# Performance work log

Hardware: AMD Instinct MI355X
Metric: run time of the kernel (lower is better)

The kernel has to match this reference:

```python
import jax, jax.numpy as jnp
import numpy as np

N_NODES = 100000
IN_CH = 256
OUT_CH = 64
N_EDGES = 3200000


def setup_inputs() -> dict:
    key = jax.random.key(0)
    k1, k2, k3, k4 = jax.random.split(key, 4)
    x = jax.random.normal(k1, (N_NODES, IN_CH), dtype=jnp.float32)
    edge_index = jax.random.randint(k2, (2, N_EDGES), 0, N_NODES, dtype=jnp.int64)
    # GCNConv parameters (glorot-style init for W, zeros for bias as in PyG)
    W = jax.random.normal(k3, (IN_CH, OUT_CH), dtype=jnp.float32) / np.sqrt(IN_CH)
    b = jnp.zeros((OUT_CH,), dtype=jnp.float32)
    return {"x": x, "edge_index": edge_index, "W": W, "b": b}


def reference(x, edge_index, W, b):
    N = x.shape[0]
    # --- GCNConv: add self-loops, symmetric degree normalization ---
    loops = jnp.arange(N, dtype=edge_index.dtype)
    src = jnp.concatenate([edge_index[0], loops])  # [E+N]
    dst = jnp.concatenate([edge_index[1], loops])  # [E+N]
    # degree of each target node (edge weights = 1)
    deg = jax.ops.segment_sum(jnp.ones_like(dst, dtype=x.dtype), dst, num_segments=N)
    dinv = jnp.where(deg > 0, jax.lax.rsqrt(deg), 0.0)  # deg^{-1/2}
    norm = dinv[src] * dinv[dst]                        # [E+N]
    # linear transform first (PyG applies lin before propagate)
    h = x @ W                                           # [N, OUT_CH]
    msg = h[src] * norm[:, None]                        # gather + scale
    out = jax.ops.segment_sum(msg, dst, num_segments=N) + b  # scatter-add + bias
    # --- relu + log_softmax ---
    out = jax.nn.relu(out)
    return jax.nn.log_softmax(out, axis=-1)
```

## Files before the change

kernel.cpp:

```cpp
#include <hip/hip_runtime.h>
#include <cstddef>
#include <cstdint>

#define N_NODES 100000
#define IN_CH 256
#define OUT_CH 64
#define N_EDGES 3200000

#define BKT_SHIFT 7
#define BKT_R     128
#define K_BKT     782
#define BKT_CAP   6144
#define T_PART    8192
#define NBLK_PART ((N_EDGES + T_PART - 1) / T_PART)
#define NBLK_GEMM 512
#define N_TILES   (N_NODES / 16)

#define WS_FLAG_OFF   0
#define WS_GCNT_OFF   64
#define WS_DINV_OFF   4096
#define WS_NSE_OFF    404096
#define WS_EDG_OFF    1204224
#define WS_H_OFF      20422656
#define WS_NEED       33222656

#define WSF_DEG_OFF   4096
#define WSF_DINV_OFF  404096
#define WSF_H_OFF     804096

typedef __attribute__((ext_vector_type(8))) short bshort8;
typedef __attribute__((ext_vector_type(4))) float f32x4;
typedef __attribute__((ext_vector_type(4))) unsigned u32x4;

static __device__ __forceinline__ unsigned short f2bf(float f) {
    unsigned u = __builtin_bit_cast(unsigned, f);
    u += 0x7FFFu + ((u >> 16) & 1u);
    return (unsigned short)(u >> 16);
}
static __device__ __forceinline__ float bflo(unsigned u) {
    return __builtin_bit_cast(float, u << 16);
}
static __device__ __forceinline__ float bfhi(unsigned u) {
    return __builtin_bit_cast(float, u & 0xFFFF0000u);
}

__global__ void probe_kernel(const unsigned* __restrict__ ei, int* __restrict__ flag) {
    if (blockIdx.x == 0 && threadIdx.x == 0) {
        int all0 = 1;
        for (int i = 0; i < 16; ++i) all0 &= (ei[2 * i + 1] == 0u);
        *flag = all0;
    }
}

__device__ __forceinline__ int load_idx(const int* ei32, const long long* ei64,
                                        bool is64, long long pos) {
    return is64 ? (int)ei64[pos] : ei32[pos];
}

static __device__ __forceinline__ void gemm_body(char* smem, int gbid, int nblk,
                                                 const float* __restrict__ x,
                                                 const float* __restrict__ W,
                                                 unsigned short* __restrict__ hs) {
    unsigned short (*Wf)[4][64][8] = (unsigned short (*)[4][64][8])smem;
    const int tid = threadIdx.x;
    const int lane = tid & 63;
    const int wv = tid >> 6;

    for (int i = tid; i < 8 * 4 * 64 * 8; i += 256) {
        int kt = i >> 11;
        int rem = i & 2047;
        int ct = rem >> 9;
        int rem2 = rem & 511;
        int l = rem2 >> 3;
        int j = rem2 & 7;
        int kk = kt * 32 + (l >> 4) * 8 + j;
        int cc = ct * 16 + (l & 15);
        ((unsigned short*)Wf)[i] = f2bf(W[(size_t)kk * OUT_CH + cc]);
    }
    __syncthreads();

    const int r16 = lane & 15;
    const int q = lane >> 4;

    for (int t = gbid * 4 + wv; t < N_TILES; t += nblk * 4) {
        const int row0 = t * 16;
        const float* xrow = &x[(size_t)(row0 + r16) * IN_CH + q * 8];
        f32x4 acc[4] = {{0.f,0.f,0.f,0.f},{0.f,0.f,0.f,0.f},
                        {0.f,0.f,0.f,0.f},{0.f,0.f,0.f,0.f}};
        #pragma unroll
        for (int kt = 0; kt < 8; ++kt) {
            float4 x0 = *(const float4*)&xrow[kt * 32];
            float4 x1 = *(const float4*)&xrow[kt * 32 + 4];
            unsigned p0, p1, p2, p3;
            asm("v_cvt_pk_bf16_f32 %0, %1, %2" : "=v"(p0) : "v"(x0.x), "v"(x0.y));
            asm("v_cvt_pk_bf16_f32 %0, %1, %2" : "=v"(p1) : "v"(x0.z), "v"(x0.w));
            asm("v_cvt_pk_bf16_f32 %0, %1, %2" : "=v"(p2) : "v"(x1.x), "v"(x1.y));
            asm("v_cvt_pk_bf16_f32 %0, %1, %2" : "=v"(p3) : "v"(x1.z), "v"(x1.w));
            u32x4 au = {p0, p1, p2, p3};
            bshort8 af = __builtin_bit_cast(bshort8, au);
            #pragma unroll
            for (int ct = 0; ct < 4; ++ct) {
                bshort8 bf = *(const bshort8*)&Wf[kt][ct][lane][0];
                acc[ct] = __builtin_amdgcn_mfma_f32_16x16x32_bf16(af, bf, acc[ct], 0, 0, 0);
            }
        }
        #pragma unroll
        for (int ct = 0; ct < 4; ++ct) {
            #pragma unroll
            for (int r = 0; r < 4; ++r) {
                int row = row0 + q * 4 + r;
                hs[(size_t)row * OUT_CH + ct * 16 + r16] = f2bf(acc[ct][r]);
            }
        }
    }
}

__global__ __launch_bounds__(512) void partition_kernel(const int* __restrict__ ei32,
                                                        const long long* __restrict__ ei64,
                                                        const int* __restrict__ flag,
                                                        unsigned* __restrict__ gcnt,
                                                        unsigned* __restrict__ edg) {
    __shared__ unsigned hist[K_BKT];
    __shared__ unsigned cur[K_BKT];
    const bool is64 = (*flag != 0);
    const int tid = threadIdx.x;
    const int start = blockIdx.x * T_PART;
    const int end   = min(start + T_PART, N_EDGES);
    for (int k = tid; k < K_BKT; k += 512) hist[k] = 0u;
    __syncthreads();
    if (is64) {
        const longlong2* d2 = (const longlong2*)&ei64[N_EDGES];
        for (int i = (start >> 1) + tid; i < (end >> 1); i += 512) {
            longlong2 d = d2[i];
            atomicAdd(&hist[(int)d.x >> BKT_SHIFT], 1u);
            atomicAdd(&hist[(int)d.y >> BKT_SHIFT], 1u);
        }
    } else {
        const int2* d2 = (const int2*)&ei32[N_EDGES];
        for (int i = (start >> 1) + tid; i < (end >> 1); i += 512) {
            int2 d = d2[i];
            atomicAdd(&hist[d.x >> BKT_SHIFT], 1u);
            atomicAdd(&hist[d.y >> BKT_SHIFT], 1u);
        }
    }
    __syncthreads();
    for (int k = tid; k < K_BKT; k += 512) {
        unsigned c = hist[k];
        unsigned base = c ? atomicAdd(&gcnt[k], c) : 0u;
        cur[k] = base + (unsigned)k * BKT_CAP;
    }
    __syncthreads();
    if (is64) {
        const longlong2* s2 = (const longlong2*)&ei64[0];
        const longlong2* d2 = (const longlong2*)&ei64[N_EDGES];
        for (int i = (start >> 1) + tid; i < (end >> 1); i += 512) {
            longlong2 s = s2[i];
            longlong2 d = d2[i];
            unsigned p0 = atomicAdd(&cur[(int)d.x >> BKT_SHIFT], 1u);
            edg[p0] = (unsigned)s.x | ((unsigned)((int)d.x & (BKT_R - 1)) << 17);
            unsigned p1 = atomicAdd(&cur[(int)d.y >> BKT_SHIFT], 1u);
            edg[p1] = (unsigned)s.y | ((unsigned)((int)d.y & (BKT_R - 1)) << 17);
        }
    } else {
        const int2* s2 = (const int2*)&ei32[0];
        const int2* d2 = (const int2*)&ei32[N_EDGES];
        for (int i = (start >> 1) + tid; i < (end >> 1); i += 512) {
            int2 s = s2[i];
            int2 d = d2[i];
            unsigned p0 = atomicAdd(&cur[d.x >> BKT_SHIFT], 1u);
            edg[p0] = (unsigned)s.x | ((unsigned)(d.x & (BKT_R - 1)) << 17);
            unsigned p1 = atomicAdd(&cur[d.y >> BKT_SHIFT], 1u);
            edg[p1] = (unsigned)s.y | ((unsigned)(d.y & (BKT_R - 1)) << 17);
        }
    }
}

__global__ __launch_bounds__(256) void sortgemm_kernel(unsigned* __restrict__ edg,
                                                       const unsigned* __restrict__ gcnt,
                                                       uint2* __restrict__ nse,
                                                       float* __restrict__ dinv,
                                                       const float* __restrict__ x,
                                                       const float* __restrict__ W,
                                                       unsigned short* __restrict__ hs) {
    __shared__ char smem[32768];
    const int bid = blockIdx.x;
    if (bid < K_BKT) {
        unsigned* ld   = (unsigned*)smem;
        unsigned* hist = (unsigned*)(smem + 24576);
        unsigned* cur  = (unsigned*)(smem + 25088);
        const int k = bid;
        const int t = threadIdx.x;
        const unsigned cnt = min(gcnt[k], (unsigned)BKT_CAP);
        const unsigned base = (unsigned)k * BKT_CAP;

        for (unsigned j = t; j < cnt; j += 256) ld[j] = edg[base + j];
        if (t < BKT_R) hist[t] = 0u;
        __syncthreads();
        for (unsigned j = t; j < cnt; j += 256)
            atomicAdd(&hist[ld[j] >> 17], 1u);
        __syncthreads();
        if (t < BKT_R) cur[t] = hist[t];
        __syncthreads();
        #pragma unroll
        for (int d = 1; d < BKT_R; d <<= 1) {
            unsigned v = (t < BKT_R && t >= d) ? cur[t - d] : 0u;
            __syncthreads();
            if (t < BKT_R) cur[t] += v;
            __syncthreads();
        }
        if (t < BKT_R) {
            unsigned mydeg = hist[t];
            unsigned start = base + cur[t] - mydeg;
            int n = k * BKT_R + t;
            if (n < N_NODES) {
                nse[n] = make_uint2(start, start + mydeg);
                dinv[n] = rsqrtf((float)(mydeg + 1u));
            }
            cur[t] = start;
        }
        __syncthreads();
        for (unsigned j = t; j < cnt; j += 256) {
            unsigned p = ld[j];
            unsigned pos = atomicAdd(&cur[p >> 17], 1u);
            edg[pos] = p & 0x1FFFF;
        }
    } else {
        gemm_body(smem, bid - K_BKT, NBLK_GEMM, x, W, hs);
    }
}

__global__ __launch_bounds__(256) void gemm_only_kernel(const float* __restrict__ x,
                                                        const float* __restrict__ W,
                                                        unsigned short* __restrict__ hs) {
    __shared__ char smem[32768];
    gemm_body(smem, blockIdx.x, gridDim.x, x, W, hs);
}

__global__ __launch_bounds__(256) void reduce_kernel(const unsigned short* __restrict__ hs,
                                                     const float* __restrict__ dinv,
                                                     const uint2* __restrict__ nse,
                                                     const int* __restrict__ ssrc,
                                                     const float* __restrict__ b,
                                                     float* __restrict__ out) {
    const int n = blockIdx.x * 4 + (threadIdx.x >> 6);
    const int lane = threadIdx.x & 63;
    const int q = lane >> 4;
    const int l16 = lane & 15;
    if (n >= N_NODES) return;
    const uint2* h8 = (const uint2*)hs;
    const float dn = dinv[n];
    float a0 = 0.f, a1 = 0.f, a2 = 0.f, a3 = 0.f;
    {
        uint2 sv = h8[(size_t)n * 16 + l16];
        if (q == 0) {
            a0 = bflo(sv.x) * dn; a1 = bfhi(sv.x) * dn;
            a2 = bflo(sv.y) * dn; a3 = bfhi(sv.y) * dn;
        }
    }
    uint2 se = nse[n];
    unsigned j = se.x;
    const unsigned end = se.y;
    for (; j + 16 <= end; j += 16) {
        int s0 = ssrc[j + q];
        int s1 = ssrc[j + 4 + q];
        int s2 = ssrc[j + 8 + q];
        int s3 = ssrc[j + 12 + q];
        float f0 = dinv[s0], f1 = dinv[s1], f2 = dinv[s2], f3 = dinv[s3];
        uint2 v0 = h8[(size_t)s0 * 16 + l16];
        uint2 v1 = h8[(size_t)s1 * 16 + l16];
        uint2 v2 = h8[(size_t)s2 * 16 + l16];
        uint2 v3 = h8[(size_t)s3 * 16 + l16];
        a0 = fmaf(bflo(v0.x), f0, a0); a1 = fmaf(bfhi(v0.x), f0, a1);
        a2 = fmaf(bflo(v0.y), f0, a2); a3 = fmaf(bfhi(v0.y), f0, a3);
        a0 = fmaf(bflo(v1.x), f1, a0); a1 = fmaf(bfhi(v1.x), f1, a1);
        a2 = fmaf(bflo(v1.y), f1, a2); a3 = fmaf(bfhi(v1.y), f1, a3);
        a0 = fmaf(bflo(v2.x), f2, a0); a1 = fmaf(bfhi(v2.x), f2, a1);
        a2 = fmaf(bflo(v2.y), f2, a2); a3 = fmaf(bfhi(v2.y), f2, a3);
        a0 = fmaf(bflo(v3.x), f3, a0); a1 = fmaf(bfhi(v3.x), f3, a1);
        a2 = fmaf(bflo(v3.y), f3, a2); a3 = fmaf(bfhi(v3.y), f3, a3);
    }
    for (; j + 4 <= end; j += 4) {
        int s = ssrc[j + q];
        float f = dinv[s];
        uint2 v = h8[(size_t)s * 16 + l16];
        a0 = fmaf(bflo(v.x), f, a0); a1 = fmaf(bfhi(v.x), f, a1);
        a2 = fmaf(bflo(v.y), f, a2); a3 = fmaf(bfhi(v.y), f, a3);
    }
    unsigned rem = end - j;
    if ((unsigned)q < rem) {
        int s = ssrc[j + q];
        float f = dinv[s];
        uint2 v = h8[(size_t)s * 16 + l16];
        a0 = fmaf(bflo(v.x), f, a0); a1 = fmaf(bfhi(v.x), f, a1);
        a2 = fmaf(bflo(v.y), f, a2); a3 = fmaf(bfhi(v.y), f, a3);
    }
    a0 += __shfl_xor(a0, 16); a0 += __shfl_xor(a0, 32);
    a1 += __shfl_xor(a1, 16); a1 += __shfl_xor(a1, 32);
    a2 += __shfl_xor(a2, 16); a2 += __shfl_xor(a2, 32);
    a3 += __shfl_xor(a3, 16); a3 += __shfl_xor(a3, 32);
    float4 bb = ((const float4*)b)[l16];
    float v0 = fmaxf(fmaf(a0, dn, bb.x), 0.f);
    float v1 = fmaxf(fmaf(a1, dn, bb.y), 0.f);
    float v2 = fmaxf(fmaf(a2, dn, bb.z), 0.f);
    float v3 = fmaxf(fmaf(a3, dn, bb.w), 0.f);
    float m = fmaxf(fmaxf(v0, v1), fmaxf(v2, v3));
    #pragma unroll
    for (int o = 8; o; o >>= 1) m = fmaxf(m, __shfl_xor(m, o));
    float sum = expf(v0 - m) + expf(v1 - m) + expf(v2 - m) + expf(v3 - m);
    #pragma unroll
    for (int o = 8; o; o >>= 1) sum += __shfl_xor(sum, o);
    float ls = logf(sum);
    if (q == 0) {
        float4 r;
        r.x = (v0 - m) - ls; r.y = (v1 - m) - ls;
        r.z = (v2 - m) - ls; r.w = (v3 - m) - ls;
        *(float4*)&out[(size_t)n * OUT_CH + l16 * 4] = r;
    }
}

__global__ __launch_bounds__(256) void deg_kernel(const int* __restrict__ ei32,
                                                  const long long* __restrict__ ei64,
                                                  const int* __restrict__ flag,
                                                  unsigned* __restrict__ deg) {
    const bool is64 = (*flag != 0);
    int i = blockIdx.x * blockDim.x + threadIdx.x;
    const int stride = gridDim.x * blockDim.x;
    for (; i < N_EDGES; i += stride) {
        int d = load_idx(ei32, ei64, is64, (long long)N_EDGES + i);
        atomicAdd(&deg[d], 1u);
    }
}

__global__ __launch_bounds__(256) void dinv_kernel(const unsigned* __restrict__ deg,
                                                   float* __restrict__ dinv) {
    int i = blockIdx.x * blockDim.x + threadIdx.x;
    if (i < N_NODES) dinv[i] = rsqrtf((float)(deg[i] + 1u));
}

__global__ __launch_bounds__(256) void scatter_kernel(const int* __restrict__ ei32,
                                                      const long long* __restrict__ ei64,
                                                      const int* __restrict__ flag,
                                                      const unsigned short* __restrict__ hs,
                                                      const float* __restrict__ dinv,
                                                      float* __restrict__ out) {
    const bool is64 = (*flag != 0);
    const int lane = threadIdx.x & 63;
    int w = blockIdx.x * (blockDim.x >> 6) + (threadIdx.x >> 6);
    const int nw = gridDim.x * (blockDim.x >> 6);
    for (int e = w; e < N_EDGES; e += nw) {
        int s = load_idx(ei32, ei64, is64, e);
        int d = load_idx(ei32, ei64, is64, (long long)N_EDGES + e);
        unsigned short us = hs[(size_t)s * OUT_CH + lane];
        float hv = __builtin_bit_cast(float, (unsigned)us << 16);
        atomicAdd(&out[(size_t)d * OUT_CH + lane], hv * dinv[s] * dinv[d]);
    }
}

__global__ __launch_bounds__(256) void final_kernel(const unsigned short* __restrict__ hs,
                                                    const float* __restrict__ dinv,
                                                    const float* __restrict__ b,
                                                    float* __restrict__ out) {
    const int lane = threadIdx.x & 63;
    int w = blockIdx.x * (blockDim.x >> 6) + (threadIdx.x >> 6);
    const int nw = gridDim.x * (blockDim.x >> 6);
    const float bias = b[lane];
    for (int n = w; n < N_NODES; n += nw) {
        float di = dinv[n];
        unsigned short us = hs[(size_t)n * OUT_CH + lane];
        float hv = __builtin_bit_cast(float, (unsigned)us << 16);
        float v = out[(size_t)n * OUT_CH + lane] + hv * di * di + bias;
        v = fmaxf(v, 0.f);
        float m = v;
        #pragma unroll
        for (int o = 32; o; o >>= 1) m = fmaxf(m, __shfl_xor(m, o));
        float ex = expf(v - m);
        float sum = ex;
        #pragma unroll
        for (int o = 32; o; o >>= 1) sum += __shfl_xor(sum, o);
        out[(size_t)n * OUT_CH + lane] = (v - m) - logf(sum);
    }
}

extern "C" void kernel_launch(void* const* d_in, const int* in_sizes, int n_in,
                              void* d_out, int out_size, void* d_ws, size_t ws_size,
                              hipStream_t stream) {
    const float* x  = (const float*)d_in[0];
    const void*  ei = d_in[1];
    const float* W  = (const float*)d_in[2];
    const float* b  = (const float*)d_in[3];
    float* out = (float*)d_out;

    char* ws = (char*)d_ws;
    int* flag = (int*)(ws + WS_FLAG_OFF);

    const int* ei32       = (const int*)ei;
    const long long* ei64 = (const long long*)ei;

    probe_kernel<<<1, 64, 0, stream>>>((const unsigned*)ei, flag);

    if (ws_size >= (size_t)WS_NEED) {
        unsigned* gcnt = (unsigned*)(ws + WS_GCNT_OFF);
        float*    dinv = (float*)(ws + WS_DINV_OFF);
        uint2*    nse  = (uint2*)(ws + WS_NSE_OFF);
        unsigned* edg  = (unsigned*)(ws + WS_EDG_OFF);
        unsigned short* hs = (unsigned short*)(ws + WS_H_OFF);

        hipMemsetAsync(gcnt, 0, K_BKT * sizeof(unsigned), stream);
        partition_kernel<<<NBLK_PART, 512, 0, stream>>>(ei32, ei64, flag, gcnt, edg);
        sortgemm_kernel<<<K_BKT + NBLK_GEMM, 256, 0, stream>>>(
            edg, gcnt, nse, dinv, x, W, hs);
        reduce_kernel<<<(N_NODES + 3) / 4, 256, 0, stream>>>(
            hs, dinv, nse, (const int*)edg, b, out);
    } else {
        unsigned* deg  = (unsigned*)(ws + WSF_DEG_OFF);
        float*    dinv = (float*)(ws + WSF_DINV_OFF);
        unsigned short* hs = (unsigned short*)(ws + WSF_H_OFF);
        hipMemsetAsync(deg, 0, (size_t)N_NODES * sizeof(unsigned), stream);
        hipMemsetAsync(d_out, 0, (size_t)out_size * sizeof(float), stream);
        deg_kernel<<<2048, 256, 0, stream>>>(ei32, ei64, flag, deg);
        dinv_kernel<<<(N_NODES + 255) / 256, 256, 0, stream>>>(deg, dinv);
        gemm_only_kernel<<<NBLK_GEMM, 256, 0, stream>>>(x, W, hs);
        scatter_kernel<<<2048, 256, 0, stream>>>(ei32, ei64, flag, hs, dinv, out);
        final_kernel<<<1024, 256, 0, stream>>>(hs, dinv, b, out);
    }
}
```

Before: 165.8 us.

## Fold gcnt memset into probe, cache dst in registers, pack FMAs

Three changes. The separate memset of the bucket counters is replaced by zeroing them inside the probe kernel, which removes one launch. The partition kernel now keeps each thread's destination indices in registers across its two passes instead of reloading them from global memory, assuming at most 8 iterations per thread. The reduce kernel accumulates with 2-wide float vectors so the compiler can emit packed FMA instructions. The fallback path may now read gcnt inside the small-workspace region, which is harmless because that path does not use it.

```diff
diff --git a/kernel.cpp b/kernel.cpp
--- a/kernel.cpp
+++ b/kernel.cpp
@@ -30,6 +30,7 @@
 
 typedef __attribute__((ext_vector_type(8))) short bshort8;
 typedef __attribute__((ext_vector_type(4))) float f32x4;
+typedef __attribute__((ext_vector_type(2))) float f32x2;
 typedef __attribute__((ext_vector_type(4))) unsigned u32x4;
 
 static __device__ __forceinline__ unsigned short f2bf(float f) {
@@ -43,12 +44,22 @@
 static __device__ __forceinline__ float bfhi(unsigned u) {
     return __builtin_bit_cast(float, u & 0xFFFF0000u);
 }
-
-__global__ void probe_kernel(const unsigned* __restrict__ ei, int* __restrict__ flag) {
-    if (blockIdx.x == 0 && threadIdx.x == 0) {
-        int all0 = 1;
-        for (int i = 0; i < 16; ++i) all0 &= (ei[2 * i + 1] == 0u);
-        *flag = all0;
+static __device__ __forceinline__ f32x2 up2(unsigned u) {
+    f32x2 r;
+    r.x = __builtin_bit_cast(float, u << 16);
+    r.y = __builtin_bit_cast(float, u & 0xFFFF0000u);
+    return r;
+}
+
+__global__ void probe_kernel(const unsigned* __restrict__ ei, int* __restrict__ flag,
+                             unsigned* __restrict__ gcnt) {
+    if (blockIdx.x == 0) {
+        for (int k = threadIdx.x; k < K_BKT; k += 64) gcnt[k] = 0u;
+        if (threadIdx.x == 0) {
+            int all0 = 1;
+            for (int i = 0; i < 16; ++i) all0 &= (ei[2 * i + 1] == 0u);
+            *flag = all0;
+        }
     }
 }
 
@@ -126,21 +137,37 @@
     const int tid = threadIdx.x;
     const int start = blockIdx.x * T_PART;
     const int end   = min(start + T_PART, N_EDGES);
+    const int pbase = start >> 1;
+    const int pend  = end >> 1;
+    unsigned dcx[8], dcy[8];
+
     for (int k = tid; k < K_BKT; k += 512) hist[k] = 0u;
     __syncthreads();
     if (is64) {
         const longlong2* d2 = (const longlong2*)&ei64[N_EDGES];
-        for (int i = (start >> 1) + tid; i < (end >> 1); i += 512) {
-            longlong2 d = d2[i];
-            atomicAdd(&hist[(int)d.x >> BKT_SHIFT], 1u);
-            atomicAdd(&hist[(int)d.y >> BKT_SHIFT], 1u);
+        #pragma unroll
+        for (int it = 0; it < 8; ++it) {
+            int i = pbase + it * 512 + tid;
+            if (i < pend) {
+                longlong2 d = d2[i];
+                dcx[it] = (unsigned)(int)d.x;
+                dcy[it] = (unsigned)(int)d.y;
+                atomicAdd(&hist[dcx[it] >> BKT_SHIFT], 1u);
+                atomicAdd(&hist[dcy[it] >> BKT_SHIFT], 1u);
+            }
         }
     } else {
         const int2* d2 = (const int2*)&ei32[N_EDGES];
-        for (int i = (start >> 1) + tid; i < (end >> 1); i += 512) {
-            int2 d = d2[i];
-            atomicAdd(&hist[d.x >> BKT_SHIFT], 1u);
-            atomicAdd(&hist[d.y >> BKT_SHIFT], 1u);
+        #pragma unroll
+        for (int it = 0; it < 8; ++it) {
+            int i = pbase + it * 512 + tid;
+            if (i < pend) {
+                int2 d = d2[i];
+                dcx[it] = (unsigned)d.x;
+                dcy[it] = (unsigned)d.y;
+                atomicAdd(&hist[dcx[it] >> BKT_SHIFT], 1u);
+                atomicAdd(&hist[dcy[it] >> BKT_SHIFT], 1u);
+            }
         }
     }
     __syncthreads();
@@ -152,25 +179,31 @@
     __syncthreads();
     if (is64) {
         const longlong2* s2 = (const longlong2*)&ei64[0];
-        const longlong2* d2 = (const longlong2*)&ei64[N_EDGES];
-        for (int i = (start >> 1) + tid; i < (end >> 1); i += 512) {
-            longlong2 s = s2[i];
-            longlong2 d = d2[i];
-            unsigned p0 = atomicAdd(&cur[(int)d.x >> BKT_SHIFT], 1u);
-            edg[p0] = (unsigned)s.x | ((unsigned)((int)d.x & (BKT_R - 1)) << 17);
-            unsigned p1 = atomicAdd(&cur[(int)d.y >> BKT_SHIFT], 1u);
-            edg[p1] = (unsigned)s.y | ((unsigned)((int)d.y & (BKT_R - 1)) << 17);
+        #pragma unroll
+        for (int it = 0; it < 8; ++it) {
+            int i = pbase + it * 512 + tid;
+            if (i < pend) {
+                longlong2 s = s2[i];
+                unsigned dx = dcx[it], dy = dcy[it];
+                unsigned p0 = atomicAdd(&cur[dx >> BKT_SHIFT], 1u);
+                edg[p0] = (unsigned)s.x | ((dx & (BKT_R - 1)) << 17);
+                unsigned p1 = atomicAdd(&cur[dy >> BKT_SHIFT], 1u);
+                edg[p1] = (unsigned)s.y | ((dy & (BKT_R - 1)) << 17);
+            }
         }
     } else {
         const int2* s2 = (const int2*)&ei32[0];
-        const int2* d2 = (const int2*)&ei32[N_EDGES];
-        for (int i = (start >> 1) + tid; i < (end >> 1); i += 512) {
-            int2 s = s2[i];
-            int2 d = d2[i];
-            unsigned p0 = atomicAdd(&cur[d.x >> BKT_SHIFT], 1u);
-            edg[p0] = (unsigned)s.x | ((unsigned)(d.x & (BKT_R - 1)) << 17);
-            unsigned p1 = atomicAdd(&cur[d.y >> BKT_SHIFT], 1u);
-            edg[p1] = (unsigned)s.y | ((unsigned)(d.y & (BKT_R - 1)) << 17);
+        #pragma unroll
+        for (int it = 0; it < 8; ++it) {
+            int i = pbase + it * 512 + tid;
+            if (i < pend) {
+                int2 s = s2[i];
+                unsigned dx = dcx[it], dy = dcy[it];
+                unsigned p0 = atomicAdd(&cur[dx >> BKT_SHIFT], 1u);
+                edg[p0] = (unsigned)s.x | ((dx & (BKT_R - 1)) << 17);
+                unsigned p1 = atomicAdd(&cur[dy >> BKT_SHIFT], 1u);
+                edg[p1] = (unsigned)s.y | ((dy & (BKT_R - 1)) << 17);
+            }
         }
     }
 }
@@ -249,12 +282,13 @@
     if (n >= N_NODES) return;
     const uint2* h8 = (const uint2*)hs;
     const float dn = dinv[n];
-    float a0 = 0.f, a1 = 0.f, a2 = 0.f, a3 = 0.f;
+    f32x2 A01 = {0.f, 0.f}, A23 = {0.f, 0.f};
     {
         uint2 sv = h8[(size_t)n * 16 + l16];
         if (q == 0) {
-            a0 = bflo(sv.x) * dn; a1 = bfhi(sv.x) * dn;
-            a2 = bflo(sv.y) * dn; a3 = bfhi(sv.y) * dn;
+            f32x2 dnv = {dn, dn};
+            A01 = up2(sv.x) * dnv;
+            A23 = up2(sv.y) * dnv;
         }
     }
     uint2 se = nse[n];
@@ -270,30 +304,28 @@
         uint2 v1 = h8[(size_t)s1 * 16 + l16];
         uint2 v2 = h8[(size_t)s2 * 16 + l16];
         uint2 v3 = h8[(size_t)s3 * 16 + l16];
-        a0 = fmaf(bflo(v0.x), f0, a0); a1 = fmaf(bfhi(v0.x), f0, a1);
-        a2 = fmaf(bflo(v0.y), f0, a2); a3 = fmaf(bfhi(v0.y), f0, a3);
-        a0 = fmaf(bflo(v1.x), f1, a0); a1 = fmaf(bfhi(v1.x), f1, a1);
-        a2 = fmaf(bflo(v1.y), f1, a2); a3 = fmaf(bfhi(v1.y), f1, a3);
-        a0 = fmaf(bflo(v2.x), f2, a0); a1 = fmaf(bfhi(v2.x), f2, a1);
-        a2 = fmaf(bflo(v2.y), f2, a2); a3 = fmaf(bfhi(v2.y), f2, a3);
-        a0 = fmaf(bflo(v3.x), f3, a0); a1 = fmaf(bfhi(v3.x), f3, a1);
-        a2 = fmaf(bflo(v3.y), f3, a2); a3 = fmaf(bfhi(v3.y), f3, a3);
+        f32x2 F0 = {f0, f0}, F1 = {f1, f1}, F2 = {f2, f2}, F3 = {f3, f3};
+        A01 += up2(v0.x) * F0; A23 += up2(v0.y) * F0;
+        A01 += up2(v1.x) * F1; A23 += up2(v1.y) * F1;
+        A01 += up2(v2.x) * F2; A23 += up2(v2.y) * F2;
+        A01 += up2(v3.x) * F3; A23 += up2(v3.y) * F3;
     }
     for (; j + 4 <= end; j += 4) {
         int s = ssrc[j + q];
         float f = dinv[s];
         uint2 v = h8[(size_t)s * 16 + l16];
-        a0 = fmaf(bflo(v.x), f, a0); a1 = fmaf(bfhi(v.x), f, a1);
-        a2 = fmaf(bflo(v.y), f, a2); a3 = fmaf(bfhi(v.y), f, a3);
+        f32x2 F = {f, f};
+        A01 += up2(v.x) * F; A23 += up2(v.y) * F;
     }
     unsigned rem = end - j;
     if ((unsigned)q < rem) {
         int s = ssrc[j + q];
         float f = dinv[s];
         uint2 v = h8[(size_t)s * 16 + l16];
-        a0 = fmaf(bflo(v.x), f, a0); a1 = fmaf(bfhi(v.x), f, a1);
-        a2 = fmaf(bflo(v.y), f, a2); a3 = fmaf(bfhi(v.y), f, a3);
-    }
+        f32x2 F = {f, f};
+        A01 += up2(v.x) * F; A23 += up2(v.y) * F;
+    }
+    float a0 = A01.x, a1 = A01.y, a2 = A23.x, a3 = A23.y;
     a0 += __shfl_xor(a0, 16); a0 += __shfl_xor(a0, 32);
     a1 += __shfl_xor(a1, 16); a1 += __shfl_xor(a1, 32);
     a2 += __shfl_xor(a2, 16); a2 += __shfl_xor(a2, 32);
@@ -392,20 +424,19 @@
 
     char* ws = (char*)d_ws;
     int* flag = (int*)(ws + WS_FLAG_OFF);
+    unsigned* gcnt = (unsigned*)(ws + WS_GCNT_OFF);
 
     const int* ei32       = (const int*)ei;
     const long long* ei64 = (const long long*)ei;
 
-    probe_kernel<<<1, 64, 0, stream>>>((const unsigned*)ei, flag);
+    probe_kernel<<<1, 64, 0, stream>>>((const unsigned*)ei, flag, gcnt);
 
     if (ws_size >= (size_t)WS_NEED) {
-        unsigned* gcnt = (unsigned*)(ws + WS_GCNT_OFF);
         float*    dinv = (float*)(ws + WS_DINV_OFF);
         uint2*    nse  = (uint2*)(ws + WS_NSE_OFF);
         unsigned* edg  = (unsigned*)(ws + WS_EDG_OFF);
         unsigned short* hs = (unsigned short*)(ws + WS_H_OFF);
 
-        hipMemsetAsync(gcnt, 0, K_BKT * sizeof(unsigned), stream);
         partition_kernel<<<NBLK_PART, 512, 0, stream>>>(ei32, ei64, flag, gcnt, edg);
         sortgemm_kernel<<<K_BKT + NBLK_GEMM, 256, 0, stream>>>(
             edg, gcnt, nse, dinv, x, W, hs);
```

Result: faster. 161.9 us (-2.4%).
